# Performance work log

Measured on AMD Instinct MI355X. Metric: run time of the kernel, lower is better.

Reference implementation:

```python
import jax, jax.numpy as jnp
import numpy as np

NEG = -1e30  # finite stand-in for -inf; exp underflows to exactly 0 in fp32


def setup_inputs() -> dict:
    key = jax.random.key(0)
    ks = jax.random.split(key, 8)
    B, L1, L2, D = 32, 2048, 512, 256
    x = jax.random.normal(ks[0], (B, L1, D), dtype=jnp.float32)
    y = jax.random.normal(ks[1], (B, L2, D), dtype=jnp.float32)
    x_mask = jax.random.randint(ks[2], (B, L1), 0, 2) > 0  # True = padding
    y_mask = jax.random.randint(ks[3], (B, L2), 0, 2) > 0
    w_x = jax.random.normal(ks[4], (D, 1), dtype=jnp.float32) * (1.0 / np.sqrt(D))
    w_y = jax.random.normal(ks[5], (D, 1), dtype=jnp.float32) * (1.0 / np.sqrt(D))
    w_dot = jax.random.normal(ks[6], (D, 1), dtype=jnp.float32) * (1.0 / np.sqrt(D))
    bias = jnp.zeros((1,), dtype=jnp.float32)
    return {"x": x, "y": y, "x_mask": x_mask, "y_mask": y_mask,
            "w_x": w_x, "w_y": w_y, "w_dot": w_dot, "bias": bias}


def reference(x, y, x_mask, y_mask, w_x, w_y, w_dot, bias):
    # trilinear BiDAF score: bias + x@w_x + y@w_y + sum_d x_d * y_d * w_dot_d
    # factorized -> no (B,L1,L2,D) intermediate, same math as xy.mm(w_dot)
    sx = x @ w_x                                    # (B, L1, 1)
    sy = jnp.swapaxes(y @ w_y, 1, 2)                # (B, 1, L2)
    sdot = jnp.einsum('bid,bjd->bij', x * w_dot[:, 0], y)  # (B, L1, L2)
    scores = bias[0] + sx + sy + sdot               # (B, L1, L2)
    scores = jnp.where(x_mask[:, :, None], NEG, scores)
    scores = jnp.where(y_mask[:, None, :], NEG, scores)

    alpha = jax.nn.softmax(scores, axis=2)          # (B, L1, L2)
    # torch code sets NaN rows (fully masked x positions) to 0
    valid_x = (~x_mask)[:, :, None].astype(x.dtype)
    alpha = alpha * valid_x
    c2q_attn = jnp.einsum('bij,bjd->bid', alpha, y)  # (B, L1, D)
    c2q_attn = c2q_attn * valid_x                    # maskzero on x padding

    beta = jax.nn.softmax(jnp.max(scores, axis=2), axis=1)  # (B, L1)
    q2c_attn = jnp.einsum('bi,bid->bd', beta, x)[:, None, :]  # (B, 1, D)

    return (c2q_attn, q2c_attn, x * c2q_attn)
```

## Files before the change

### kernel.cpp

```cpp
#include <hip/hip_runtime.h>
#include <hip/hip_bf16.h>
#include <stdint.h>

#define BB 32
#define L1 2048
#define L2 512
#define DD 256
#define L2E 1.4426950408889634f
#define NEGS (-1.0e30f * 1.4426950408889634f)

#if __has_builtin(__builtin_amdgcn_exp2f)
#define EXP2(x) __builtin_amdgcn_exp2f(x)
#else
#define EXP2(x) exp2f(x)
#endif

typedef __attribute__((ext_vector_type(4))) float f32x4;
typedef __attribute__((ext_vector_type(8))) short bf16x8;
typedef __attribute__((ext_vector_type(4))) unsigned short u16x4;
typedef __attribute__((ext_vector_type(8))) unsigned short u16x8;

__device__ __forceinline__ unsigned short f2b(float f) {
    union { __hip_bfloat16 h; unsigned short u; } cv;
    cv.h = __float2bfloat16(f);
    return cv.u;
}

__global__ void prep(const float* __restrict__ y, const float* __restrict__ w_y,
                     unsigned short* __restrict__ ybt, unsigned short* __restrict__ ytt,
                     float* __restrict__ sy) {
    __shared__ float tile[64][264];
    const int tid = threadIdx.x;
    const int lane = tid & 63;
    const int sub = tid >> 6;
    const int b = blockIdx.y;
    const int j0 = blockIdx.x * 64;
    const float* yb = y + ((size_t)b * L2 + j0) * DD;
    f32x4 wv = *(const f32x4*)(w_y + lane * 4);
    #pragma unroll
    for (int p = 0; p < 16; ++p) {
        int row = p * 4 + sub;
        f32x4 v = *(const f32x4*)(yb + (size_t)row * DD + lane * 4);
        *(f32x4*)&tile[row][lane * 4] = v;
        float s = v[0]*wv[0] + v[1]*wv[1] + v[2]*wv[2] + v[3]*wv[3];
        #pragma unroll
        for (int off = 32; off; off >>= 1) s += __shfl_xor(s, off, 64);
        if (lane == 0) sy[b * L2 + j0 + row] = s;
    }
    __syncthreads();
    #pragma unroll
    for (int it = 0; it < 8; ++it) {
        int idx = it * 256 + tid;
        int jt = idx >> 9;
        int rem = idx & 511;
        int kc = rem >> 6;
        int l = rem & 63;
        const float* tr = &tile[jt * 16 + (l & 15)][kc * 32 + (l >> 4) * 8];
        u16x8 pk;
        #pragma unroll
        for (int e = 0; e < 8; ++e) pk[e] = f2b(tr[e]);
        size_t off = (((size_t)b * 32 + blockIdx.x * 4 + jt) * 8 + kc) * 512 + l * 8;
        *(u16x8*)(ybt + off) = pk;
    }
    #pragma unroll
    for (int it = 0; it < 8; ++it) {
        int idx = it * 256 + tid;
        int dt = idx >> 7;
        int rem = idx & 127;
        int kk = rem >> 6;
        int l = rem & 63;
        int c = l & 15, g = l >> 4;
        u16x8 pk;
        #pragma unroll
        for (int e = 0; e < 8; ++e) pk[e] = f2b(tile[kk * 32 + g * 8 + e][dt * 16 + c]);
        size_t off = (((size_t)b * 16 + dt) * 16 + blockIdx.x * 2 + kk) * 512 + l * 8;
        *(u16x8*)(ytt + off) = pk;
    }
}

__launch_bounds__(256, 2)
__global__ void attn_main(const float* __restrict__ x,
                          const unsigned short* __restrict__ ybt,
                          const unsigned short* __restrict__ ytt,
                          const float* __restrict__ sy,
                          const float* __restrict__ w_x,
                          const float* __restrict__ w_dot,
                          const float* __restrict__ bias,
                          const int* __restrict__ x_mask,
                          const int* __restrict__ y_mask,
                          float* __restrict__ out0,
                          float* __restrict__ out2,
                          float* __restrict__ part,
                          float* __restrict__ MbA,
                          float* __restrict__ SeA) {
    __shared__ __align__(16) unsigned short big[32768];
    __shared__ float sxs[64];
    __shared__ int   xms[64];
    __shared__ float pmax[4][64];
    __shared__ float pz[4][64];

    const int tid = threadIdx.x;
    const int w = tid >> 6;
    const int lane = tid & 63;
    const int g = lane >> 4, c = lane & 15;

    const int wg = blockIdx.x;
    const int slot = wg >> 3;
    const int b = (wg & 7) * 4 + (slot >> 5);
    const int rowblk = slot & 31;
    const int i0 = rowblk * 64;

    {
        const int arow = w * 16 + c;
        const float* xrow = x + ((size_t)(b * L1 + i0 + arow)) * DD;
        float sxpart = 0.f;
        #pragma unroll
        for (int kb = 0; kb < 8; ++kb) {
            int koff = kb * 32 + g * 8;
            f32x4 lo = *(const f32x4*)(xrow + koff);
            f32x4 hi = *(const f32x4*)(xrow + koff + 4);
            f32x4 wdlo = *(const f32x4*)(w_dot + koff);
            f32x4 wdhi = *(const f32x4*)(w_dot + koff + 4);
            f32x4 wxlo = *(const f32x4*)(w_x + koff);
            f32x4 wxhi = *(const f32x4*)(w_x + koff + 4);
            u16x8 a;
            #pragma unroll
            for (int e = 0; e < 4; ++e) {
                a[e]     = f2b(lo[e] * wdlo[e]);
                a[e + 4] = f2b(hi[e] * wdhi[e]);
                sxpart += lo[e] * wxlo[e] + hi[e] * wxhi[e];
            }
            int u = (kb * 4 + g) ^ (c & 7);
            *(u16x8*)((char*)big + arow * 512 + u * 16) = a;
        }
        sxpart += __shfl_xor(sxpart, 16, 64);
        sxpart += __shfl_xor(sxpart, 32, 64);
        if (g == 0) {
            int xmv = x_mask[b * L1 + i0 + arow];
            xms[arow] = xmv;
            sxs[arow] = xmv ? NEGS : (sxpart + bias[0]) * L2E;
        }
    }
    __syncthreads();

    f32x4 S[4][8];
    #pragma unroll
    for (int mt = 0; mt < 4; ++mt)
        #pragma unroll
        for (int nt = 0; nt < 8; ++nt) S[mt][nt] = (f32x4){0.f, 0.f, 0.f, 0.f};

    const unsigned short* ybt_b = ybt + (size_t)b * 131072;
    const int col0 = w * 128;
    #pragma unroll 2
    for (int ck = 0; ck < 8; ++ck) {
        bf16x8 bfr[8];
        #pragma unroll
        for (int nt = 0; nt < 8; ++nt)
            bfr[nt] = *(const bf16x8*)(ybt_b + ((size_t)((w * 8 + nt) * 8 + ck) * 512) + lane * 8);
        bf16x8 afr[4];
        #pragma unroll
        for (int mt = 0; mt < 4; ++mt)
            afr[mt] = *(const bf16x8*)((char*)big + (mt * 16 + c) * 512 + ((((ck * 4 + g)) ^ (c & 7)) << 4));
        #pragma unroll
        for (int mt = 0; mt < 4; ++mt)
            #pragma unroll
            for (int nt = 0; nt < 8; ++nt)
                S[mt][nt] = __builtin_amdgcn_mfma_f32_16x16x32_bf16(afr[mt], bfr[nt], S[mt][nt], 0, 0, 0);
    }

    float syt[8];
    #pragma unroll
    for (int nt = 0; nt < 8; ++nt) {
        float sv = sy[b * L2 + col0 + nt * 16 + c];
        int ym = y_mask[b * L2 + col0 + nt * 16 + c];
        syt[nt] = ym ? NEGS : sv * L2E;
    }
    float sxr[4][4]; int xmr[4][4];
    #pragma unroll
    for (int mt = 0; mt < 4; ++mt)
        #pragma unroll
        for (int r = 0; r < 4; ++r) {
            sxr[mt][r] = sxs[mt * 16 + 4 * g + r];
            xmr[mt][r] = xms[mt * 16 + 4 * g + r];
        }
    #pragma unroll
    for (int mt = 0; mt < 4; ++mt)
        #pragma unroll
        for (int nt = 0; nt < 8; ++nt)
            #pragma unroll
            for (int r = 0; r < 4; ++r)
                S[mt][nt][r] = fmaf(S[mt][nt][r], L2E, sxr[mt][r]) + syt[nt];

    #pragma unroll
    for (int mt = 0; mt < 4; ++mt)
        #pragma unroll
        for (int r = 0; r < 4; ++r) {
            float pm = S[mt][0][r];
            #pragma unroll
            for (int nt = 1; nt < 8; ++nt) pm = fmaxf(pm, S[mt][nt][r]);
            pm = fmaxf(pm, __shfl_xor(pm, 1, 64));
            pm = fmaxf(pm, __shfl_xor(pm, 2, 64));
            pm = fmaxf(pm, __shfl_xor(pm, 4, 64));
            pm = fmaxf(pm, __shfl_xor(pm, 8, 64));
            if (c == 0) pmax[w][mt * 16 + 4 * g + r] = pm;
        }
    __syncthreads();
    float mrow[4][4];
    #pragma unroll
    for (int mt = 0; mt < 4; ++mt)
        #pragma unroll
        for (int r = 0; r < 4; ++r) {
            int row = mt * 16 + 4 * g + r;
            mrow[mt][r] = fmaxf(fmaxf(pmax[0][row], pmax[1][row]),
                                fmaxf(pmax[2][row], pmax[3][row]));
        }
    #pragma unroll
    for (int mt = 0; mt < 4; ++mt)
        #pragma unroll
        for (int r = 0; r < 4; ++r) {
            float zp = 0.f;
            #pragma unroll
            for (int nt = 0; nt < 8; ++nt) {
                float e = EXP2(S[mt][nt][r] - mrow[mt][r]);
                S[mt][nt][r] = e;
                zp += e;
            }
            zp += __shfl_xor(zp, 1, 64);
            zp += __shfl_xor(zp, 2, 64);
            zp += __shfl_xor(zp, 4, 64);
            zp += __shfl_xor(zp, 8, 64);
            if (c == 0) pz[w][mt * 16 + 4 * g + r] = zp;
        }
    __syncthreads();
    float zinv[4][4];
    #pragma unroll
    for (int mt = 0; mt < 4; ++mt)
        #pragma unroll
        for (int r = 0; r < 4; ++r) {
            int row = mt * 16 + 4 * g + r;
            zinv[mt][r] = 1.f / ((pz[0][row] + pz[1][row]) + (pz[2][row] + pz[3][row]));
        }

    float Mb;
    {
        float t = mrow[0][0];
        #pragma unroll
        for (int mt = 0; mt < 4; ++mt)
            #pragma unroll
            for (int r = 0; r < 4; ++r) t = fmaxf(t, mrow[mt][r]);
        t = fmaxf(t, __shfl_xor(t, 16, 64));
        t = fmaxf(t, __shfl_xor(t, 32, 64));
        Mb = t;
    }
    float ev[4][4];
    float Se = 0.f;
    #pragma unroll
    for (int mt = 0; mt < 4; ++mt)
        #pragma unroll
        for (int r = 0; r < 4; ++r) {
            ev[mt][r] = EXP2(mrow[mt][r] - Mb);
            Se += ev[mt][r];
        }
    Se += __shfl_xor(Se, 16, 64);
    Se += __shfl_xor(Se, 32, 64);
    if (tid == 0) {
        MbA[b * 32 + rowblk] = Mb;
        SeA[b * 32 + rowblk] = Se;
    }

    #pragma unroll
    for (int mt = 0; mt < 4; ++mt)
        #pragma unroll
        for (int nt = 0; nt < 8; ++nt)
            #pragma unroll
            for (int r = 0; r < 4; ++r) {
                int row = mt * 16 + 4 * g + r;
                int col = col0 + nt * 16 + c;
                *(unsigned short*)((char*)big + row * 1024 +
                                   (((col >> 3) ^ (row & 7)) << 4) + (col & 7) * 2)
                    = f2b(S[mt][nt][r]);
            }
    __syncthreads();

    f32x4 o[4][4];
    #pragma unroll
    for (int mt = 0; mt < 4; ++mt)
        #pragma unroll
        for (int nt = 0; nt < 4; ++nt) o[mt][nt] = (f32x4){0.f, 0.f, 0.f, 0.f};
    const unsigned short* ytt_b = ytt + (size_t)b * 131072;
    #pragma unroll 4
    for (int kf = 0; kf < 16; ++kf) {
        bf16x8 bv[4];
        #pragma unroll
        for (int nt = 0; nt < 4; ++nt)
            bv[nt] = *(const bf16x8*)(ytt_b + ((size_t)((w * 4 + nt) * 16 + kf) * 512) + lane * 8);
        bf16x8 av[4];
        #pragma unroll
        for (int mt = 0; mt < 4; ++mt)
            av[mt] = *(const bf16x8*)((char*)big + (mt * 16 + c) * 1024 + ((((kf * 4 + g)) ^ (c & 7)) << 4));
        #pragma unroll
        for (int mt = 0; mt < 4; ++mt)
            #pragma unroll
            for (int nt = 0; nt < 4; ++nt)
                o[mt][nt] = __builtin_amdgcn_mfma_f32_16x16x32_bf16(av[mt], bv[nt], o[mt][nt], 0, 0, 0);
    }

    const float* xb2 = x + ((size_t)b * L1 + i0) * DD;
    const size_t outb = ((size_t)b * L1 + i0) * DD;
    float eq[4] = {0.f, 0.f, 0.f, 0.f};
    #pragma unroll
    for (int mt = 0; mt < 4; ++mt)
        #pragma unroll
        for (int r = 0; r < 4; ++r) {
            int row = mt * 16 + 4 * g + r;
            float zi = zinv[mt][r];
            float ee = ev[mt][r];
            int xmv = xmr[mt][r];
            #pragma unroll
            for (int nt = 0; nt < 4; ++nt) {
                int d = w * 64 + nt * 16 + c;
                float xv = xb2[(size_t)row * DD + d];
                float cv = xmv ? 0.f : o[mt][nt][r] * zi;
                out0[outb + (size_t)row * DD + d] = cv;
                out2[outb + (size_t)row * DD + d] = xv * cv;
                eq[nt] = fmaf(ee, xv, eq[nt]);
            }
        }
    #pragma unroll
    for (int nt = 0; nt < 4; ++nt) {
        float v = eq[nt];
        v += __shfl_xor(v, 16, 64);
        v += __shfl_xor(v, 32, 64);
        if (g == 0) part[((size_t)(b * 32 + rowblk)) * DD + w * 64 + nt * 16 + c] = v;
    }
}

__global__ void q2c_combine(const float* __restrict__ part, const float* __restrict__ MbA,
                            const float* __restrict__ SeA, float* __restrict__ out1) {
    int b = blockIdx.x, d = threadIdx.x;
    float M = -3.0e38f;
    #pragma unroll
    for (int k = 0; k < 32; ++k) M = fmaxf(M, MbA[b * 32 + k]);
    float Z = 0.f, s = 0.f;
    #pragma unroll 8
    for (int k = 0; k < 32; ++k) {
        float wk = exp2f(MbA[b * 32 + k] - M);
        Z += SeA[b * 32 + k] * wk;
        s += part[((size_t)(b * 32 + k)) * DD + d] * wk;
    }
    out1[b * DD + d] = s / Z;
}

extern "C" void kernel_launch(void* const* d_in, const int* in_sizes, int n_in,
                              void* d_out, int out_size, void* d_ws, size_t ws_size,
                              hipStream_t stream) {
    const float* x = (const float*)d_in[0];
    const float* y = (const float*)d_in[1];
    const int* x_mask = (const int*)d_in[2];
    const int* y_mask = (const int*)d_in[3];
    const float* w_x = (const float*)d_in[4];
    const float* w_y = (const float*)d_in[5];
    const float* w_dot = (const float*)d_in[6];
    const float* bias = (const float*)d_in[7];

    char* ws = (char*)d_ws;
    unsigned short* ybt = (unsigned short*)ws;
    unsigned short* ytt = (unsigned short*)(ws + 8388608);
    float* sy   = (float*)(ws + 16777216);
    float* part = (float*)(ws + 16842752);
    float* MbA  = (float*)(ws + 17891328);
    float* SeA  = (float*)(ws + 17895424);

    float* out0 = (float*)d_out;
    float* out1 = out0 + (size_t)BB * L1 * DD;
    float* out2 = out1 + (size_t)BB * DD;

    prep<<<dim3(L2 / 64, BB), 256, 0, stream>>>(y, w_y, ybt, ytt, sy);
    attn_main<<<dim3(BB * L1 / 64), 256, 0, stream>>>(x, ybt, ytt, sy, w_x, w_dot, bias,
                                                      x_mask, y_mask, out0, out2,
                                                      part, MbA, SeA);
    q2c_combine<<<dim3(BB), 256, 0, stream>>>(part, MbA, SeA, out1);
}
```

Before: 106.7 us.

## Double-buffer global B-fragment loads in both MFMA loops and relax launch bounds

Software-pipelines the y-fragment global loads in both the score GEMM and the output GEMM. Each iteration prefetches the next k-slice into a second register buffer, and the first slice is issued before the x staging and the softmax phase. Both loops are fully unrolled, and launch bounds drop to one block per CU minimum so the compiler can use the extra registers. The aim is to hide global-load latency behind MFMA work, at the cost of register pressure and possibly lower occupancy.

```diff
diff --git a/kernel.cpp b/kernel.cpp
--- a/kernel.cpp
+++ b/kernel.cpp
@@ -78,7 +78,7 @@
     }
 }
 
-__launch_bounds__(256, 2)
+__launch_bounds__(256, 1)
 __global__ void attn_main(const float* __restrict__ x,
                           const unsigned short* __restrict__ ybt,
                           const unsigned short* __restrict__ ytt,
@@ -110,6 +110,14 @@
     const int rowblk = slot & 31;
     const int i0 = rowblk * 64;
 
+    const unsigned short* ybt_b = ybt + (size_t)b * 131072;
+    const int col0 = w * 128;
+
+    bf16x8 bfrA[8], bfrB[8];
+    #pragma unroll
+    for (int nt = 0; nt < 8; ++nt)
+        bfrA[nt] = *(const bf16x8*)(ybt_b + ((size_t)((w * 8 + nt) * 8 + 0) * 512) + lane * 8);
+
     {
         const int arow = w * 16 + c;
         const float* xrow = x + ((size_t)(b * L1 + i0 + arow)) * DD;
@@ -149,14 +157,19 @@
         #pragma unroll
         for (int nt = 0; nt < 8; ++nt) S[mt][nt] = (f32x4){0.f, 0.f, 0.f, 0.f};
 
-    const unsigned short* ybt_b = ybt + (size_t)b * 131072;
-    const int col0 = w * 128;
-    #pragma unroll 2
+    #pragma unroll
     for (int ck = 0; ck < 8; ++ck) {
-        bf16x8 bfr[8];
-        #pragma unroll
-        for (int nt = 0; nt < 8; ++nt)
-            bfr[nt] = *(const bf16x8*)(ybt_b + ((size_t)((w * 8 + nt) * 8 + ck) * 512) + lane * 8);
+        if (ck < 7) {
+            if (ck & 1) {
+                #pragma unroll
+                for (int nt = 0; nt < 8; ++nt)
+                    bfrA[nt] = *(const bf16x8*)(ybt_b + ((size_t)((w * 8 + nt) * 8 + ck + 1) * 512) + lane * 8);
+            } else {
+                #pragma unroll
+                for (int nt = 0; nt < 8; ++nt)
+                    bfrB[nt] = *(const bf16x8*)(ybt_b + ((size_t)((w * 8 + nt) * 8 + ck + 1) * 512) + lane * 8);
+            }
+        }
         bf16x8 afr[4];
         #pragma unroll
         for (int mt = 0; mt < 4; ++mt)
@@ -165,8 +178,15 @@
         for (int mt = 0; mt < 4; ++mt)
             #pragma unroll
             for (int nt = 0; nt < 8; ++nt)
-                S[mt][nt] = __builtin_amdgcn_mfma_f32_16x16x32_bf16(afr[mt], bfr[nt], S[mt][nt], 0, 0, 0);
-    }
+                S[mt][nt] = __builtin_amdgcn_mfma_f32_16x16x32_bf16(
+                    afr[mt], (ck & 1) ? bfrB[nt] : bfrA[nt], S[mt][nt], 0, 0, 0);
+    }
+
+    const unsigned short* ytt_b = ytt + (size_t)b * 131072;
+    bf16x8 bvA[4], bvB[4];
+    #pragma unroll
+    for (int nt = 0; nt < 4; ++nt)
+        bvA[nt] = *(const bf16x8*)(ytt_b + ((size_t)((w * 4 + nt) * 16 + 0) * 512) + lane * 8);
 
     float syt[8];
     #pragma unroll
@@ -287,13 +307,19 @@
     for (int mt = 0; mt < 4; ++mt)
         #pragma unroll
         for (int nt = 0; nt < 4; ++nt) o[mt][nt] = (f32x4){0.f, 0.f, 0.f, 0.f};
-    const unsigned short* ytt_b = ytt + (size_t)b * 131072;
-    #pragma unroll 4
+    #pragma unroll
     for (int kf = 0; kf < 16; ++kf) {
-        bf16x8 bv[4];
-        #pragma unroll
-        for (int nt = 0; nt < 4; ++nt)
-            bv[nt] = *(const bf16x8*)(ytt_b + ((size_t)((w * 4 + nt) * 16 + kf) * 512) + lane * 8);
+        if (kf < 15) {
+            if (kf & 1) {
+                #pragma unroll
+                for (int nt = 0; nt < 4; ++nt)
+                    bvA[nt] = *(const bf16x8*)(ytt_b + ((size_t)((w * 4 + nt) * 16 + kf + 1) * 512) + lane * 8);
+            } else {
+                #pragma unroll
+                for (int nt = 0; nt < 4; ++nt)
+                    bvB[nt] = *(const bf16x8*)(ytt_b + ((size_t)((w * 4 + nt) * 16 + kf + 1) * 512) + lane * 8);
+            }
+        }
         bf16x8 av[4];
         #pragma unroll
         for (int mt = 0; mt < 4; ++mt)
@@ -302,7 +328,8 @@
         for (int mt = 0; mt < 4; ++mt)
             #pragma unroll
             for (int nt = 0; nt < 4; ++nt)
-                o[mt][nt] = __builtin_amdgcn_mfma_f32_16x16x32_bf16(av[mt], bv[nt], o[mt][nt], 0, 0, 0);
+                o[mt][nt] = __builtin_amdgcn_mfma_f32_16x16x32_bf16(
+                    av[mt], (kf & 1) ? bvB[nt] : bvA[nt], o[mt][nt], 0, 0, 0);
     }
 
     const float* xb2 = x + ((size_t)b * L1 + i0) * DD;
```

Result: slower. 134.5 us (+26.1%).
